# Kernel optimization log

Measured on AMD Instinct MI355X. Metric: run time of the kernel, lower is better.

Reference implementation:

```python
import jax, jax.numpy as jnp
import numpy as np

B, S, D = 2, 2048, 4096
H, KV, HD = 32, 8, 128
THETA = 500000.0


def setup_inputs() -> dict:
    key = jax.random.key(0)
    ks = jax.random.split(key, 5)
    x = jax.random.normal(ks[0], (B, S, D), jnp.float32) * 0.02
    wq = jax.random.normal(ks[1], (H * HD, D), jnp.float32) * 0.02
    wk = jax.random.normal(ks[2], (KV * HD, D), jnp.float32) * 0.02
    wv = jax.random.normal(ks[3], (KV * HD, D), jnp.float32) * 0.02
    wo = jax.random.normal(ks[4], (D, H * HD), jnp.float32) * 0.02
    # HF-style rotary embeddings: cos/sin of shape [B, S, head_dim]
    inv_freq = 1.0 / (THETA ** (jnp.arange(0, HD, 2, dtype=jnp.float32) / HD))
    pos = jnp.arange(S, dtype=jnp.float32)
    freqs = pos[:, None] * inv_freq[None, :]            # [S, HD/2]
    emb = jnp.concatenate([freqs, freqs], axis=-1)      # [S, HD]
    cos = jnp.broadcast_to(jnp.cos(emb)[None], (B, S, HD)).astype(jnp.float32)
    sin = jnp.broadcast_to(jnp.sin(emb)[None], (B, S, HD)).astype(jnp.float32)
    return {"x": x, "wq": wq, "wk": wk, "wv": wv, "wo": wo, "cos": cos, "sin": sin}


def _rotate_half(u):
    return jnp.concatenate([-u[..., HD // 2:], u[..., :HD // 2]], axis=-1)


def reference(x, wq, wk, wv, wo, cos, sin):
    # QKV projections (Linear with weight [out, in], bias=False)
    q = (x @ wq.T).reshape(B, S, H, HD).transpose(0, 2, 1, 3)    # [B,H,S,HD]
    k = (x @ wk.T).reshape(B, S, KV, HD).transpose(0, 2, 1, 3)   # [B,KV,S,HD]
    v = (x @ wv.T).reshape(B, S, KV, HD).transpose(0, 2, 1, 3)   # [B,KV,S,HD]
    # RoPE (rotate_half convention), cos/sin broadcast over heads
    c = cos[:, None, :, :]
    s = sin[:, None, :, :]
    q = q * c + _rotate_half(q) * s
    k = k * c + _rotate_half(k) * s
    # GQA: repeat kv heads
    rep = H // KV
    k = jnp.repeat(k, rep, axis=1)
    v = jnp.repeat(v, rep, axis=1)
    # causal SDPA (attention_mask=None, q_len>1 -> is_causal=True)
    scores = jnp.einsum('bhqd,bhkd->bhqk', q, k) / jnp.sqrt(jnp.float32(HD))
    causal = jnp.tril(jnp.ones((S, S), dtype=bool))
    scores = jnp.where(causal[None, None], scores, jnp.float32(-1e30))
    probs = jax.nn.softmax(scores, axis=-1)
    attn = jnp.einsum('bhqk,bhkd->bhqd', probs, v)
    attn = attn.transpose(0, 2, 1, 3).reshape(B, S, H * HD)
    return attn @ wo.T
```

## Files before the change

kernel.cpp:

```cpp
#include <hip/hip_runtime.h>
#include <hip/hip_bf16.h>

#define B_ 2
#define S_ 2048
#define D_ 4096
#define H_ 32
#define KV_ 8
#define HD_ 128

typedef __attribute__((ext_vector_type(8))) short sh8;
typedef __attribute__((ext_vector_type(4))) float f32x4;

__device__ __forceinline__ float b2f(unsigned short u) {
    union { unsigned int i; float f; } v; v.i = ((unsigned)u) << 16; return v.f;
}
__device__ __forceinline__ unsigned short f2b(float f) {
    union { float f; unsigned int i; } v; v.f = f;
    unsigned r = v.i + 0x7fffu + ((v.i >> 16) & 1u);
    return (unsigned short)(r >> 16);
}
__device__ __forceinline__ void gload_lds16(const void* g, void* l) {
    __builtin_amdgcn_global_load_lds((const __attribute__((address_space(1))) void*)g,
                                     (__attribute__((address_space(3))) void*)l, 16, 0, 0);
}

#define BARX() do { asm volatile("" ::: "memory"); __builtin_amdgcn_s_barrier(); asm volatile("" ::: "memory"); } while (0)

__global__ __launch_bounds__(256) void f2b_kernel(const float* __restrict__ in,
                                                  unsigned short* __restrict__ out, int n8) {
    int t = blockIdx.x * 256 + threadIdx.x;
    if (t >= n8) return;
    const float* p = in + (size_t)t * 8;
    float4 a = *(const float4*)p;
    float4 b = *(const float4*)(p + 4);
    sh8 o;
    o[0] = (short)f2b(a.x); o[1] = (short)f2b(a.y); o[2] = (short)f2b(a.z); o[3] = (short)f2b(a.w);
    o[4] = (short)f2b(b.x); o[5] = (short)f2b(b.y); o[6] = (short)f2b(b.z); o[7] = (short)f2b(b.w);
    *(sh8*)(out + (size_t)t * 8) = o;
}

__device__ __forceinline__ void cstore(float* C, size_t i, float v) { C[i] = v; }
__device__ __forceinline__ void cstore(unsigned short* C, size_t i, float v) { C[i] = f2b(v); }

template <typename CT>
__global__ __launch_bounds__(256) void gemm_bt_kernel(const unsigned short* __restrict__ A,
                                                      const unsigned short* __restrict__ Bm,
                                                      CT* __restrict__ C, int M, int N, int K) {
    __shared__ __align__(16) unsigned short As[128 * 32];
    __shared__ __align__(16) unsigned short Bs[128 * 32];
    int nwg = gridDim.x;
    int wg = blockIdx.x;
    int cpx = nwg >> 3;
    int swz = (wg & 7) * cpx + (wg >> 3);
    int nbn = N >> 7;
    int bm = swz / nbn, bn = swz % nbn;
    int t = threadIdx.x, w = t >> 6, l = t & 63;
    int wm = w >> 1, wn = w & 1;
    int fr = l & 15, fq = l >> 4;
    f32x4 acc[4][4];
#pragma unroll
    for (int i = 0; i < 4; i++)
#pragma unroll
        for (int j = 0; j < 4; j++) acc[i][j] = (f32x4){0.f, 0.f, 0.f, 0.f};
    const size_t rowA0 = (size_t)bm * 128, rowB0 = (size_t)bn * 128;
    int lrow = l >> 2;
    int lcb = (l & 3) * 16;
    for (int k0 = 0; k0 < K; k0 += 32) {
#pragma unroll
        for (int r = 0; r < 2; ++r) {
            int chunk = r * 4 + w;
            int row = chunk * 16 + lrow;
            const char* ga = (const char*)(A + (rowA0 + row) * (size_t)K + k0) + lcb;
            gload_lds16(ga, (char*)As + chunk * 1024);
            const char* gb = (const char*)(Bm + (rowB0 + row) * (size_t)K + k0) + lcb;
            gload_lds16(gb, (char*)Bs + chunk * 1024);
        }
        __syncthreads();
        sh8 af[4], bfv[4];
#pragma unroll
        for (int mi = 0; mi < 4; mi++) af[mi] = *(const sh8*)(As + (wm * 64 + mi * 16 + fr) * 32 + fq * 8);
#pragma unroll
        for (int ni = 0; ni < 4; ni++) bfv[ni] = *(const sh8*)(Bs + (wn * 64 + ni * 16 + fr) * 32 + fq * 8);
#pragma unroll
        for (int mi = 0; mi < 4; mi++)
#pragma unroll
            for (int ni = 0; ni < 4; ni++)
                acc[mi][ni] = __builtin_amdgcn_mfma_f32_16x16x32_bf16(af[mi], bfv[ni], acc[mi][ni], 0, 0, 0);
        __syncthreads();
    }
#pragma unroll
    for (int mi = 0; mi < 4; mi++)
#pragma unroll
        for (int ni = 0; ni < 4; ni++) {
            size_t row = rowA0 + wm * 64 + mi * 16 + fq * 4;
            size_t col = rowB0 + wn * 64 + ni * 16 + fr;
#pragma unroll
            for (int j = 0; j < 4; j++) cstore(C, (row + j) * (size_t)N + col, acc[mi][ni][j]);
        }
}

#define MFMAQ(MH, NH)                                                                              \
    do {                                                                                           \
        __builtin_amdgcn_s_setprio(1);                                                             \
        _Pragma("unroll") for (int ks = 0; ks < 2; ks++)                                           \
        _Pragma("unroll") for (int mi = 0; mi < 4; mi++)                                           \
        _Pragma("unroll") for (int ni = 0; ni < 2; ni++)                                           \
            acc[(MH)*4 + mi][(NH)*2 + ni] = __builtin_amdgcn_mfma_f32_16x16x32_bf16(               \
                af[mi][ks], bfr[ni][ks], acc[(MH)*4 + mi][(NH)*2 + ni], 0, 0, 0);                  \
        __builtin_amdgcn_s_setprio(0);                                                             \
    } while (0)

__device__ __forceinline__ void stage2(const unsigned short* s, size_t off128, int tp,
                                       unsigned short* d) {
    const unsigned short* sp = s + (size_t)tp * 64;
    gload_lds16(sp, d);
    gload_lds16(sp + off128, d + 4096);
}

template <typename CT>
__global__ __launch_bounds__(512, 2) void gemm256_bt_kernel(const unsigned short* __restrict__ A,
                                                            const unsigned short* __restrict__ Bm,
                                                            CT* __restrict__ C, int M, int N, int K) {
    __shared__ __align__(16) unsigned short Al[2][2][8192];
    __shared__ __align__(16) unsigned short Bl[2][2][8192];
    const int NT = K >> 6;
    const int nwg = gridDim.x;
    const int wg = blockIdx.x;
    const int cpx = nwg >> 3;
    const int swz = (wg & 7) * cpx + (wg >> 3);
    const int nbn = N >> 8;
    const int bm = swz / nbn, bn = swz % nbn;
    const int T = threadIdx.x;
    const int w = T >> 6, l = T & 63;
    const int wm = w >> 2, wn = w & 3;
    const int fr = l & 15, fq = l >> 4;
    const int u = T >> 3;
    const int swc = ((T & 7) ^ (u & 7)) << 3;
    const size_t Ks = (size_t)K;
    const size_t off128 = 128 * Ks;
    const unsigned short* a0s = A + ((size_t)bm * 256 + u) * Ks + swc;
    const unsigned short* a1s = A + ((size_t)bm * 256 + 64 + u) * Ks + swc;
    const unsigned short* b0s = Bm + ((size_t)bn * 256 + (u >> 5) * 64 + (u & 31)) * Ks + swc;
    const unsigned short* b1s = b0s + 32 * Ks;
    const int T8 = T * 8;
    int aoff[4][2], boff[2][2];
#pragma unroll
    for (int mi = 0; mi < 4; mi++)
#pragma unroll
        for (int ks = 0; ks < 2; ks++)
            aoff[mi][ks] = (wm * 64 + mi * 16 + fr) * 64 + ((((ks << 2) | fq) ^ (fr & 7)) << 3);
#pragma unroll
    for (int ni = 0; ni < 2; ni++)
#pragma unroll
        for (int ks = 0; ks < 2; ks++)
            boff[ni][ks] = (wn * 32 + ni * 16 + fr) * 64 + ((((ks << 2) | fq) ^ (fr & 7)) << 3);
    f32x4 acc[8][4];
#pragma unroll
    for (int i = 0; i < 8; i++)
#pragma unroll
        for (int j = 0; j < 4; j++) acc[i][j] = (f32x4){0.f, 0.f, 0.f, 0.f};

    stage2(a0s, off128, 0, &Al[0][0][T8]);
    stage2(a1s, off128, 0, &Al[0][1][T8]);
    stage2(b0s, off128, 0, &Bl[0][0][T8]);
    stage2(b1s, off128, 0, &Bl[0][1][T8]);
    const int t1c = (NT > 1) ? 1 : 0;
    stage2(a0s, off128, t1c, &Al[1][0][T8]);
    stage2(b1s, off128, t1c, &Bl[1][1][T8]);
    asm volatile("s_waitcnt vmcnt(4)" ::: "memory");
    BARX();

    sh8 af[4][2], bfr[2][2];
    for (int t = 0; t < NT; ++t) {
        const int p = t & 1, pn = p ^ 1;
        const int tp1 = (t + 1 < NT) ? t + 1 : NT - 1;
        const int tp2 = (t + 2 < NT) ? t + 2 : NT - 1;
        const unsigned short* Am0 = &Al[p][0][0];
        const unsigned short* Am1 = &Al[p][1][0];
        const unsigned short* Bn0 = &Bl[p][0][0];
        const unsigned short* Bn1 = &Bl[p][1][0];
#pragma unroll
        for (int mi = 0; mi < 4; mi++) {
            af[mi][0] = *(const sh8*)(Am0 + aoff[mi][0]);
            af[mi][1] = *(const sh8*)(Am0 + aoff[mi][1]);
        }
#pragma unroll
        for (int ni = 0; ni < 2; ni++) {
            bfr[ni][0] = *(const sh8*)(Bn0 + boff[ni][0]);
            bfr[ni][1] = *(const sh8*)(Bn0 + boff[ni][1]);
        }
        stage2(a1s, off128, tp1, &Al[pn][1][T8]);
        BARX();
        MFMAQ(0, 0);
        BARX();
#pragma unroll
        for (int ni = 0; ni < 2; ni++) {
            bfr[ni][0] = *(const sh8*)(Bn1 + boff[ni][0]);
            bfr[ni][1] = *(const sh8*)(Bn1 + boff[ni][1]);
        }
        stage2(b0s, off128, tp1, &Bl[pn][0][T8]);
        BARX();
        MFMAQ(0, 1);
        BARX();
#pragma unroll
        for (int mi = 0; mi < 4; mi++) {
            af[mi][0] = *(const sh8*)(Am1 + aoff[mi][0]);
            af[mi][1] = *(const sh8*)(Am1 + aoff[mi][1]);
        }
        stage2(a0s, off128, tp2, &Al[p][0][T8]);
        BARX();
        MFMAQ(1, 1);
        BARX();
#pragma unroll
        for (int ni = 0; ni < 2; ni++) {
            bfr[ni][0] = *(const sh8*)(Bn0 + boff[ni][0]);
            bfr[ni][1] = *(const sh8*)(Bn0 + boff[ni][1]);
        }
        stage2(b1s, off128, tp2, &Bl[p][1][T8]);
        asm volatile("s_waitcnt vmcnt(4)" ::: "memory");
        BARX();
        MFMAQ(1, 0);
        BARX();
    }
    const size_t crow0 = (size_t)bm * 256 + wm * 128;
    const size_t ccol0 = (size_t)bn * 256 + wn * 64;
#pragma unroll
    for (int mi8 = 0; mi8 < 8; mi8++)
#pragma unroll
        for (int ni4 = 0; ni4 < 4; ni4++) {
            size_t r = crow0 + mi8 * 16 + fq * 4;
            size_t c = ccol0 + ni4 * 16 + fr;
#pragma unroll
            for (int j = 0; j < 4; j++) cstore(C, (r + j) * (size_t)N + c, acc[mi8][ni4][j]);
        }
}

template <int NH>
__global__ __launch_bounds__(256) void rope_kernel(const unsigned short* __restrict__ raw,
                                                   const float* __restrict__ cosb,
                                                   const float* __restrict__ sinb,
                                                   unsigned short* __restrict__ out, float scale) {
    int t = blockIdx.x * 256 + threadIdx.x;
    int g = t & 7;
    int h = (t >> 3) & (NH - 1);
    int row = t / (8 * NH);
    if (row >= B_ * S_) return;
    int b = row >> 11, s = row & (S_ - 1);
    const unsigned short* qr = raw + (size_t)row * (NH * HD_) + h * HD_ + g * 8;
    sh8 lo = *(const sh8*)qr;
    sh8 hi = *(const sh8*)(qr + 64);
    const float* cp = cosb + (size_t)row * HD_ + g * 8;
    const float* sp = sinb + (size_t)row * HD_ + g * 8;
    float4 c0 = *(const float4*)cp, c1 = *(const float4*)(cp + 4);
    float4 s0 = *(const float4*)sp, s1 = *(const float4*)(sp + 4);
    float cc[8] = {c0.x, c0.y, c0.z, c0.w, c1.x, c1.y, c1.z, c1.w};
    float ss[8] = {s0.x, s0.y, s0.z, s0.w, s1.x, s1.y, s1.z, s1.w};
    sh8 olo, ohi;
#pragma unroll
    for (int i = 0; i < 8; i++) {
        float fl = b2f((unsigned short)lo[i]);
        float fh = b2f((unsigned short)hi[i]);
        olo[i] = (short)f2b((fl * cc[i] - fh * ss[i]) * scale);
        ohi[i] = (short)f2b((fh * cc[i] + fl * ss[i]) * scale);
    }
    unsigned short* op = out + (((size_t)b * NH + h) * S_ + s) * HD_ + g * 8;
    *(sh8*)op = olo;
    *(sh8*)(op + 64) = ohi;
}

__global__ __launch_bounds__(256) void vtrans_kernel(const unsigned short* __restrict__ vraw,
                                                     unsigned short* __restrict__ vt) {
    __shared__ unsigned short tile[64][132];
    int bid = blockIdx.x;
    int st = bid & 31;
    int kv = (bid >> 5) & 7;
    int b = bid >> 8;
    int s0 = st * 64;
    int t = threadIdx.x;
    {
        int s = t >> 2, dq = (t & 3) * 32;
        const unsigned short* src = vraw + ((size_t)(b * S_ + s0 + s)) * (KV_ * HD_) + kv * HD_ + dq;
#pragma unroll
        for (int i = 0; i < 4; i++) *(sh8*)&tile[s][dq + i * 8] = *(const sh8*)(src + i * 8);
    }
    __syncthreads();
    {
        int d = t & 127, sh = t >> 7;
        unsigned short* dst = vt + (((size_t)(b * KV_ + kv)) * HD_ + d) * S_ + s0 + sh * 32;
#pragma unroll
        for (int q = 0; q < 4; q++) {
            sh8 vv;
#pragma unroll
            for (int e = 0; e < 8; e++) vv[e] = (short)tile[sh * 32 + q * 8 + e][d];
            *(sh8*)(dst + q * 8) = vv;
        }
    }
}

__global__ __launch_bounds__(256) void attn_kernel(const unsigned short* __restrict__ Q,
                                                   const unsigned short* __restrict__ Kr,
                                                   const unsigned short* __restrict__ Vt,
                                                   unsigned short* __restrict__ O) {
    __shared__ __align__(16) unsigned short Kl[64 * 128];
    __shared__ __align__(16) unsigned short Vl[128 * 64];
    __shared__ __align__(16) unsigned short Pl[4][16 * 72];
    int nwg = gridDim.x;
    int bid0 = blockIdx.x;
    int cpx = nwg >> 3;
    int u = (bid0 & 7) * cpx + (bid0 >> 3);
    int qi = u & 31;
    int h = (u >> 5) & 31;
    int b = u >> 10;
    int kv = h >> 2;
    int t = threadIdx.x, w = t >> 6, l = t & 63;
    int fr = l & 15, fq = l >> 4;
    int qw = qi * 64 + w * 16;
    const unsigned short* Qp = Q + (((size_t)b * H_ + h) * S_ + qw + fr) * HD_;
    sh8 qf[4];
#pragma unroll
    for (int kk = 0; kk < 4; kk++) qf[kk] = *(const sh8*)(Qp + kk * 32 + fq * 8);
    const unsigned short* Kg = Kr + ((size_t)b * KV_ + kv) * S_ * HD_;
    const unsigned short* Vg = Vt + ((size_t)b * KV_ + kv) * HD_ * S_;
    f32x4 po[8];
#pragma unroll
    for (int i = 0; i < 8; i++) po[i] = (f32x4){0.f, 0.f, 0.f, 0.f};
    float m_r[4] = {-3.0e38f, -3.0e38f, -3.0e38f, -3.0e38f};
    float l_r[4] = {0.f, 0.f, 0.f, 0.f};
    for (int j = 0; j <= qi; ++j) {
#pragma unroll
        for (int r = 0; r < 4; ++r) {
            int chunk = r * 4 + w;
            {
                int lb = chunk * 1024 + l * 16;
                int srow = lb >> 8;
                int cs = (lb >> 4) & 15;
                int gs = cs ^ (srow & 7);
                const char* ga = (const char*)(Kg + (size_t)(j * 64 + srow) * HD_) + gs * 16;
                gload_lds16(ga, (char*)Kl + chunk * 1024);
            }
            {
                int lb = chunk * 1024 + l * 16;
                int drow = lb >> 7;
                int cs = (lb >> 4) & 7;
                int gs = cs ^ (drow & 7);
                const char* gv = (const char*)(Vg + (size_t)drow * S_ + j * 64 + gs * 8);
                gload_lds16(gv, (char*)Vl + chunk * 1024);
            }
        }
        __syncthreads();
        f32x4 sacc[4];
#pragma unroll
        for (int nc = 0; nc < 4; nc++) {
            sacc[nc] = (f32x4){0.f, 0.f, 0.f, 0.f};
            int n = nc * 16 + fr;
#pragma unroll
            for (int kk = 0; kk < 4; kk++) {
                sh8 kf = *(const sh8*)(Kl + n * 128 + (((kk * 4 + fq) ^ (n & 7)) * 8));
                sacc[nc] = __builtin_amdgcn_mfma_f32_16x16x32_bf16(qf[kk], kf, sacc[nc], 0, 0, 0);
            }
        }
        if (j == qi) {
#pragma unroll
            for (int nc = 0; nc < 4; nc++) {
                int kg = j * 64 + nc * 16 + fr;
#pragma unroll
                for (int j3 = 0; j3 < 4; j3++) {
                    int qg = qw + fq * 4 + j3;
                    if (kg > qg) sacc[nc][j3] = -1e30f;
                }
            }
        }
        float pb[4][4];
#pragma unroll
        for (int j3 = 0; j3 < 4; j3++) {
            float tm = sacc[0][j3];
#pragma unroll
            for (int nc = 1; nc < 4; nc++) tm = fmaxf(tm, sacc[nc][j3]);
            tm = fmaxf(tm, __shfl_xor(tm, 1));
            tm = fmaxf(tm, __shfl_xor(tm, 2));
            tm = fmaxf(tm, __shfl_xor(tm, 4));
            tm = fmaxf(tm, __shfl_xor(tm, 8));
            float newm = fmaxf(m_r[j3], tm);
            float alpha = __expf(m_r[j3] - newm);
            float rs = 0.f;
#pragma unroll
            for (int nc = 0; nc < 4; nc++) {
                float p = __expf(sacc[nc][j3] - newm);
                pb[nc][j3] = p;
                rs += p;
            }
            rs += __shfl_xor(rs, 1);
            rs += __shfl_xor(rs, 2);
            rs += __shfl_xor(rs, 4);
            rs += __shfl_xor(rs, 8);
            l_r[j3] = l_r[j3] * alpha + rs;
            m_r[j3] = newm;
#pragma unroll
            for (int dc = 0; dc < 8; dc++) po[dc][j3] *= alpha;
        }
        unsigned short* Pw = Pl[w];
#pragma unroll
        for (int nc = 0; nc < 4; nc++)
#pragma unroll
            for (int j3 = 0; j3 < 4; j3++)
                Pw[(fq * 4 + j3) * 72 + nc * 16 + fr] = f2b(pb[nc][j3]);
#pragma unroll
        for (int kc = 0; kc < 2; kc++) {
            sh8 pf = *(const sh8*)(Pw + fr * 72 + kc * 32 + fq * 8);
#pragma unroll
            for (int dc = 0; dc < 8; dc++) {
                int d = dc * 16 + fr;
                sh8 vf = *(const sh8*)(Vl + d * 64 + (((kc * 4 + fq) ^ (d & 7)) * 8));
                po[dc] = __builtin_amdgcn_mfma_f32_16x16x32_bf16(pf, vf, po[dc], 0, 0, 0);
            }
        }
        __syncthreads();
    }
#pragma unroll
    for (int j3 = 0; j3 < 4; j3++) {
        float inv = 1.f / l_r[j3];
        size_t orow = (size_t)b * S_ + qw + fq * 4 + j3;
#pragma unroll
        for (int dc = 0; dc < 8; dc++)
            O[orow * (H_ * HD_) + h * HD_ + dc * 16 + fr] = f2b(po[dc][j3] * inv);
    }
}

extern "C" void kernel_launch(void* const* d_in, const int* in_sizes, int n_in,
                              void* d_out, int out_size, void* d_ws, size_t ws_size,
                              hipStream_t stream) {
    const float* x = (const float*)d_in[0];
    const float* wq = (const float*)d_in[1];
    const float* wk = (const float*)d_in[2];
    const float* wv = (const float*)d_in[3];
    const float* wo = (const float*)d_in[4];
    const float* cosb = (const float*)d_in[5];
    const float* sinb = (const float*)d_in[6];
    float* out = (float*)d_out;

    unsigned short* p = (unsigned short*)d_ws;
    unsigned short* xb = p;    p += (size_t)16777216;
    unsigned short* wqb = p;   p += (size_t)16777216;
    unsigned short* wob = p;   p += (size_t)16777216;
    unsigned short* qraw = p;  p += (size_t)16777216;
    unsigned short* qrope = p; p += (size_t)16777216;
    unsigned short* attn = p;  p += (size_t)16777216;
    unsigned short* wkb = p;   p += (size_t)4194304;
    unsigned short* wvb = p;   p += (size_t)4194304;
    unsigned short* kraw = p;  p += (size_t)4194304;
    unsigned short* vraw = p;  p += (size_t)4194304;
    unsigned short* krope = p; p += (size_t)4194304;
    unsigned short* vt = p;    p += (size_t)4194304;

    f2b_kernel<<<8192, 256, 0, stream>>>(x, xb, 2097152);
    f2b_kernel<<<8192, 256, 0, stream>>>(wq, wqb, 2097152);
    f2b_kernel<<<2048, 256, 0, stream>>>(wk, wkb, 524288);
    f2b_kernel<<<2048, 256, 0, stream>>>(wv, wvb, 524288);
    f2b_kernel<<<8192, 256, 0, stream>>>(wo, wob, 2097152);

    gemm256_bt_kernel<unsigned short><<<256, 512, 0, stream>>>(xb, wqb, qraw, 4096, 4096, 4096);
    gemm_bt_kernel<unsigned short><<<256, 256, 0, stream>>>(xb, wkb, kraw, 4096, 1024, 4096);
    gemm_bt_kernel<unsigned short><<<256, 256, 0, stream>>>(xb, wvb, vraw, 4096, 1024, 4096);

    rope_kernel<32><<<4096, 256, 0, stream>>>(qraw, cosb, sinb, qrope, 0.08838834764831845f);
    rope_kernel<8><<<1024, 256, 0, stream>>>(kraw, cosb, sinb, krope, 1.0f);
    vtrans_kernel<<<512, 256, 0, stream>>>(vraw, vt);

    attn_kernel<<<2048, 256, 0, stream>>>(qrope, krope, vt, attn);

    gemm256_bt_kernel<float><<<256, 512, 0, stream>>>(attn, wob, out, 4096, 4096, 4096);
}
```

Baseline: 940.1 us.

## Fuse QKV projections into one GEMM and keep attention P in registers

Result: faster. 827.4 us (-12.0%).

```diff
diff --git a/kernel.cpp b/kernel.cpp
--- a/kernel.cpp
+++ b/kernel.cpp
@@ -9,6 +9,7 @@
 #define HD_ 128
 
 typedef __attribute__((ext_vector_type(8))) short sh8;
+typedef __attribute__((ext_vector_type(4))) short sh4;
 typedef __attribute__((ext_vector_type(4))) float f32x4;
 
 __device__ __forceinline__ float b2f(unsigned short u) {
@@ -41,63 +42,6 @@
 
 __device__ __forceinline__ void cstore(float* C, size_t i, float v) { C[i] = v; }
 __device__ __forceinline__ void cstore(unsigned short* C, size_t i, float v) { C[i] = f2b(v); }
-
-template <typename CT>
-__global__ __launch_bounds__(256) void gemm_bt_kernel(const unsigned short* __restrict__ A,
-                                                      const unsigned short* __restrict__ Bm,
-                                                      CT* __restrict__ C, int M, int N, int K) {
-    __shared__ __align__(16) unsigned short As[128 * 32];
-    __shared__ __align__(16) unsigned short Bs[128 * 32];
-    int nwg = gridDim.x;
-    int wg = blockIdx.x;
-    int cpx = nwg >> 3;
-    int swz = (wg & 7) * cpx + (wg >> 3);
-    int nbn = N >> 7;
-    int bm = swz / nbn, bn = swz % nbn;
-    int t = threadIdx.x, w = t >> 6, l = t & 63;
-    int wm = w >> 1, wn = w & 1;
-    int fr = l & 15, fq = l >> 4;
-    f32x4 acc[4][4];
-#pragma unroll
-    for (int i = 0; i < 4; i++)
-#pragma unroll
-        for (int j = 0; j < 4; j++) acc[i][j] = (f32x4){0.f, 0.f, 0.f, 0.f};
-    const size_t rowA0 = (size_t)bm * 128, rowB0 = (size_t)bn * 128;
-    int lrow = l >> 2;
-    int lcb = (l & 3) * 16;
-    for (int k0 = 0; k0 < K; k0 += 32) {
-#pragma unroll
-        for (int r = 0; r < 2; ++r) {
-            int chunk = r * 4 + w;
-            int row = chunk * 16 + lrow;
-            const char* ga = (const char*)(A + (rowA0 + row) * (size_t)K + k0) + lcb;
-            gload_lds16(ga, (char*)As + chunk * 1024);
-            const char* gb = (const char*)(Bm + (rowB0 + row) * (size_t)K + k0) + lcb;
-            gload_lds16(gb, (char*)Bs + chunk * 1024);
-        }
-        __syncthreads();
-        sh8 af[4], bfv[4];
-#pragma unroll
-        for (int mi = 0; mi < 4; mi++) af[mi] = *(const sh8*)(As + (wm * 64 + mi * 16 + fr) * 32 + fq * 8);
-#pragma unroll
-        for (int ni = 0; ni < 4; ni++) bfv[ni] = *(const sh8*)(Bs + (wn * 64 + ni * 16 + fr) * 32 + fq * 8);
-#pragma unroll
-        for (int mi = 0; mi < 4; mi++)
-#pragma unroll
-            for (int ni = 0; ni < 4; ni++)
-                acc[mi][ni] = __builtin_amdgcn_mfma_f32_16x16x32_bf16(af[mi], bfv[ni], acc[mi][ni], 0, 0, 0);
-        __syncthreads();
-    }
-#pragma unroll
-    for (int mi = 0; mi < 4; mi++)
-#pragma unroll
-        for (int ni = 0; ni < 4; ni++) {
-            size_t row = rowA0 + wm * 64 + mi * 16 + fq * 4;
-            size_t col = rowB0 + wn * 64 + ni * 16 + fr;
-#pragma unroll
-            for (int j = 0; j < 4; j++) cstore(C, (row + j) * (size_t)N + col, acc[mi][ni][j]);
-        }
-}
 
 #define MFMAQ(MH, NH)                                                                              \
     do {                                                                                           \
@@ -239,14 +183,15 @@
 __global__ __launch_bounds__(256) void rope_kernel(const unsigned short* __restrict__ raw,
                                                    const float* __restrict__ cosb,
                                                    const float* __restrict__ sinb,
-                                                   unsigned short* __restrict__ out, float scale) {
+                                                   unsigned short* __restrict__ out, float scale,
+                                                   int srcOff, int srcStride) {
     int t = blockIdx.x * 256 + threadIdx.x;
     int g = t & 7;
     int h = (t >> 3) & (NH - 1);
     int row = t / (8 * NH);
     if (row >= B_ * S_) return;
     int b = row >> 11, s = row & (S_ - 1);
-    const unsigned short* qr = raw + (size_t)row * (NH * HD_) + h * HD_ + g * 8;
+    const unsigned short* qr = raw + (size_t)row * srcStride + srcOff + h * HD_ + g * 8;
     sh8 lo = *(const sh8*)qr;
     sh8 hi = *(const sh8*)(qr + 64);
     const float* cp = cosb + (size_t)row * HD_ + g * 8;
@@ -279,7 +224,7 @@
     int t = threadIdx.x;
     {
         int s = t >> 2, dq = (t & 3) * 32;
-        const unsigned short* src = vraw + ((size_t)(b * S_ + s0 + s)) * (KV_ * HD_) + kv * HD_ + dq;
+        const unsigned short* src = vraw + ((size_t)(b * S_ + s0 + s)) * 6144 + 5120 + kv * HD_ + dq;
 #pragma unroll
         for (int i = 0; i < 4; i++) *(sh8*)&tile[s][dq + i * 8] = *(const sh8*)(src + i * 8);
     }
@@ -297,13 +242,24 @@
     }
 }
 
-__global__ __launch_bounds__(256) void attn_kernel(const unsigned short* __restrict__ Q,
-                                                   const unsigned short* __restrict__ Kr,
-                                                   const unsigned short* __restrict__ Vt,
-                                                   unsigned short* __restrict__ O) {
+#if __has_builtin(__builtin_amdgcn_mfma_f32_16x16x16bf16_1k)
+__device__ __forceinline__ f32x4 pv_mfma(sh4 a, sh4 b, f32x4 c) {
+    return __builtin_amdgcn_mfma_f32_16x16x16bf16_1k(a, b, c, 0, 0, 0);
+}
+#else
+__device__ __forceinline__ f32x4 pv_mfma(sh4 a, sh4 b, f32x4 c) {
+    sh8 a8 = {a[0], a[1], a[2], a[3], 0, 0, 0, 0};
+    sh8 b8 = {b[0], b[1], b[2], b[3], 0, 0, 0, 0};
+    return __builtin_amdgcn_mfma_f32_16x16x32_bf16(a8, b8, c, 0, 0, 0);
+}
+#endif
+
+__global__ __launch_bounds__(256, 4) void attn_kernel(const unsigned short* __restrict__ Q,
+                                                      const unsigned short* __restrict__ Kr,
+                                                      const unsigned short* __restrict__ Vt,
+                                                      unsigned short* __restrict__ O) {
     __shared__ __align__(16) unsigned short Kl[64 * 128];
     __shared__ __align__(16) unsigned short Vl[128 * 64];
-    __shared__ __align__(16) unsigned short Pl[4][16 * 72];
     int nwg = gridDim.x;
     int bid0 = blockIdx.x;
     int cpx = nwg >> 3;
@@ -324,8 +280,8 @@
     f32x4 po[8];
 #pragma unroll
     for (int i = 0; i < 8; i++) po[i] = (f32x4){0.f, 0.f, 0.f, 0.f};
-    float m_r[4] = {-3.0e38f, -3.0e38f, -3.0e38f, -3.0e38f};
-    float l_r[4] = {0.f, 0.f, 0.f, 0.f};
+    float m_r = -3.0e38f;
+    float l_r = 0.f;
     for (int j = 0; j <= qi; ++j) {
 #pragma unroll
         for (int r = 0; r < 4; ++r) {
@@ -356,73 +312,85 @@
 #pragma unroll
             for (int kk = 0; kk < 4; kk++) {
                 sh8 kf = *(const sh8*)(Kl + n * 128 + (((kk * 4 + fq) ^ (n & 7)) * 8));
-                sacc[nc] = __builtin_amdgcn_mfma_f32_16x16x32_bf16(qf[kk], kf, sacc[nc], 0, 0, 0);
+                sacc[nc] = __builtin_amdgcn_mfma_f32_16x16x32_bf16(kf, qf[kk], sacc[nc], 0, 0, 0);
             }
         }
         if (j == qi) {
-#pragma unroll
-            for (int nc = 0; nc < 4; nc++) {
-                int kg = j * 64 + nc * 16 + fr;
+            int qg = qw + fr;
+#pragma unroll
+            for (int nc = 0; nc < 4; nc++)
 #pragma unroll
                 for (int j3 = 0; j3 < 4; j3++) {
-                    int qg = qw + fq * 4 + j3;
+                    int kg = j * 64 + nc * 16 + fq * 4 + j3;
                     if (kg > qg) sacc[nc][j3] = -1e30f;
                 }
+        }
+        float tm = sacc[0][0];
+#pragma unroll
+        for (int nc = 0; nc < 4; nc++)
+#pragma unroll
+            for (int j3 = 0; j3 < 4; j3++) tm = fmaxf(tm, sacc[nc][j3]);
+        tm = fmaxf(tm, __shfl_xor(tm, 16));
+        tm = fmaxf(tm, __shfl_xor(tm, 32));
+        bool resc = !__all(tm <= m_r + 8.0f);
+        if (resc) {
+            float nm = fmaxf(m_r, tm);
+            float alpha = __expf(m_r - nm);
+            m_r = nm;
+            l_r *= alpha;
+            float aj[4];
+#pragma unroll
+            for (int j3 = 0; j3 < 4; j3++) aj[j3] = __shfl(alpha, (l & 48) | (fq * 4 + j3));
+#pragma unroll
+            for (int dc = 0; dc < 8; dc++)
+#pragma unroll
+                for (int j3 = 0; j3 < 4; j3++) po[dc][j3] *= aj[j3];
+        }
+        float rs = 0.f;
+#pragma unroll
+        for (int nc = 0; nc < 4; nc++)
+#pragma unroll
+            for (int j3 = 0; j3 < 4; j3++) {
+                float pv = __expf(sacc[nc][j3] - m_r);
+                sacc[nc][j3] = pv;
+                rs += pv;
             }
-        }
-        float pb[4][4];
-#pragma unroll
-        for (int j3 = 0; j3 < 4; j3++) {
-            float tm = sacc[0][j3];
-#pragma unroll
-            for (int nc = 1; nc < 4; nc++) tm = fmaxf(tm, sacc[nc][j3]);
-            tm = fmaxf(tm, __shfl_xor(tm, 1));
-            tm = fmaxf(tm, __shfl_xor(tm, 2));
-            tm = fmaxf(tm, __shfl_xor(tm, 4));
-            tm = fmaxf(tm, __shfl_xor(tm, 8));
-            float newm = fmaxf(m_r[j3], tm);
-            float alpha = __expf(m_r[j3] - newm);
-            float rs = 0.f;
+        rs += __shfl_xor(rs, 16);
+        rs += __shfl_xor(rs, 32);
+        l_r += rs;
+        sh4 pa[4];
+#pragma unroll
+        for (int nc = 0; nc < 4; nc++) {
+            unsigned int lo, hi;
+            asm("v_cvt_pk_bf16_f32 %0, %1, %2" : "=v"(lo) : "v"(sacc[nc][0]), "v"(sacc[nc][1]));
+            asm("v_cvt_pk_bf16_f32 %0, %1, %2" : "=v"(hi) : "v"(sacc[nc][2]), "v"(sacc[nc][3]));
+            union { unsigned int u2[2]; sh4 v; } pk;
+            pk.u2[0] = lo; pk.u2[1] = hi;
+            pa[nc] = pk.v;
+        }
+#pragma unroll
+        for (int dc = 0; dc < 8; dc++) {
+            int d = dc * 16 + fr;
 #pragma unroll
             for (int nc = 0; nc < 4; nc++) {
-                float p = __expf(sacc[nc][j3] - newm);
-                pb[nc][j3] = p;
-                rs += p;
+                const unsigned short* vp =
+                    Vl + d * 64 + (((2 * nc + (fq >> 1)) ^ (d & 7)) * 8) + (fq & 1) * 4;
+                sh4 vf = *(const sh4*)vp;
+                po[dc] = pv_mfma(pa[nc], vf, po[dc]);
             }
-            rs += __shfl_xor(rs, 1);
-            rs += __shfl_xor(rs, 2);
-            rs += __shfl_xor(rs, 4);
-            rs += __shfl_xor(rs, 8);
-            l_r[j3] = l_r[j3] * alpha + rs;
-            m_r[j3] = newm;
-#pragma unroll
-            for (int dc = 0; dc < 8; dc++) po[dc][j3] *= alpha;
-        }
-        unsigned short* Pw = Pl[w];
-#pragma unroll
-        for (int nc = 0; nc < 4; nc++)
-#pragma unroll
-            for (int j3 = 0; j3 < 4; j3++)
-                Pw[(fq * 4 + j3) * 72 + nc * 16 + fr] = f2b(pb[nc][j3]);
-#pragma unroll
-        for (int kc = 0; kc < 2; kc++) {
-            sh8 pf = *(const sh8*)(Pw + fr * 72 + kc * 32 + fq * 8);
-#pragma unroll
-            for (int dc = 0; dc < 8; dc++) {
-                int d = dc * 16 + fr;
-                sh8 vf = *(const sh8*)(Vl + d * 64 + (((kc * 4 + fq) ^ (d & 7)) * 8));
-                po[dc] = __builtin_amdgcn_mfma_f32_16x16x32_bf16(pf, vf, po[dc], 0, 0, 0);
-            }
         }
         __syncthreads();
     }
+    float il = 1.f / l_r;
+    float inj[4];
+#pragma unroll
+    for (int j3 = 0; j3 < 4; j3++) inj[j3] = __shfl(il, (l & 48) | (fq * 4 + j3));
 #pragma unroll
     for (int j3 = 0; j3 < 4; j3++) {
-        float inv = 1.f / l_r[j3];
         size_t orow = (size_t)b * S_ + qw + fq * 4 + j3;
 #pragma unroll
         for (int dc = 0; dc < 8; dc++)
-            O[orow * (H_ * HD_) + h * HD_ + dc * 16 + fr] = f2b(po[dc][j3] * inv);
+            O[orow * (H_ * HD_) + h * HD_ + dc * 16 + fr] = f2b(po[dc][j3] * inj[j3]);
     }
 }
 
@@ -439,34 +407,28 @@
     float* out = (float*)d_out;
 
     unsigned short* p = (unsigned short*)d_ws;
-    unsigned short* xb = p;    p += (size_t)16777216;
-    unsigned short* wqb = p;   p += (size_t)16777216;
-    unsigned short* wob = p;   p += (size_t)16777216;
-    unsigned short* qraw = p;  p += (size_t)16777216;
-    unsigned short* qrope = p; p += (size_t)16777216;
-    unsigned short* attn = p;  p += (size_t)16777216;
-    unsigned short* wkb = p;   p += (size_t)4194304;
-    unsigned short* wvb = p;   p += (size_t)4194304;
-    unsigned short* kraw = p;  p += (size_t)4194304;
-    unsigned short* vraw = p;  p += (size_t)4194304;
-    unsigned short* krope = p; p += (size_t)4194304;
-    unsigned short* vt = p;    p += (size_t)4194304;
+    unsigned short* xb = p;      p += (size_t)16777216;
+    unsigned short* wqkvb = p;   p += (size_t)25165824;
+    unsigned short* wob = p;     p += (size_t)16777216;
+    unsigned short* qkvraw = p;  p += (size_t)25165824;
+    unsigned short* qrope = p;   p += (size_t)16777216;
+    unsigned short* krope = p;   p += (size_t)4194304;
+    unsigned short* vt = p;      p += (size_t)4194304;
+    unsigned short* attnb = p;   p += (size_t)16777216;
 
     f2b_kernel<<<8192, 256, 0, stream>>>(x, xb, 2097152);
-    f2b_kernel<<<8192, 256, 0, stream>>>(wq, wqb, 2097152);
-    f2b_kernel<<<2048, 256, 0, stream>>>(wk, wkb, 524288);
-    f2b_kernel<<<2048, 256, 0, stream>>>(wv, wvb, 524288);
+    f2b_kernel<<<8192, 256, 0, stream>>>(wq, wqkvb, 2097152);
+    f2b_kernel<<<2048, 256, 0, stream>>>(wk, wqkvb + (size_t)16777216, 524288);
+    f2b_kernel<<<2048, 256, 0, stream>>>(wv, wqkvb + (size_t)20971520, 524288);
     f2b_kernel<<<8192, 256, 0, stream>>>(wo, wob, 2097152);
 
-    gemm256_bt_kernel<unsigned short><<<256, 512, 0, stream>>>(xb, wqb, qraw, 4096, 4096, 4096);
-    gemm_bt_kernel<unsigned short><<<256, 256, 0, stream>>>(xb, wkb, kraw, 4096, 1024, 4096);
-    gemm_bt_kernel<unsigned short><<<256, 256, 0, stream>>>(xb, wvb, vraw, 4096, 1024, 4096);
-
-    rope_kernel<32><<<4096, 256, 0, stream>>>(qraw, cosb, sinb, qrope, 0.08838834764831845f);
-    rope_kernel<8><<<1024, 256, 0, stream>>>(kraw, cosb, sinb, krope, 1.0f);
-    vtrans_kernel<<<512, 256, 0, stream>>>(vraw, vt);
-
-    attn_kernel<<<2048, 256, 0, stream>>>(qrope, krope, vt, attn);
-
-    gemm256_bt_kernel<float><<<256, 512, 0, stream>>>(attn, wob, out, 4096, 4096, 4096);
-}
+    gemm256_bt_kernel<unsigned short><<<384, 512, 0, stream>>>(xb, wqkvb, qkvraw, 4096, 6144, 4096);
+
+    rope_kernel<32><<<4096, 256, 0, stream>>>(qkvraw, cosb, sinb, qrope, 0.08838834764831845f, 0, 6144);
+    rope_kernel<8><<<1024, 256, 0, stream>>>(qkvraw, cosb, sinb, krope, 1.0f, 4096, 6144);
+    vtrans_kernel<<<512, 256, 0, stream>>>(qkvraw, vt);
+
+    attn_kernel<<<2048, 256, 0, stream>>>(qrope, krope, vt, attnb);
+
+    gemm256_bt_kernel<float><<<256, 512, 0, stream>>>(attnb, wob, out, 4096, 4096, 4096);
+}
```
